# Kernel tuning notes

Hardware: AMD Instinct MI355X
Metric: run time of the kernel (lower is better)

## Reference

```python
import jax, jax.numpy as jnp
import numpy as np

DIM = 1024
HEADS = 16


def setup_inputs() -> dict:
    key = jax.random.key(0)
    ks = jax.random.split(key, 8)
    b, n, d = 2, 2048, DIM
    x = jax.random.normal(ks[0], (b, n, d), dtype=jnp.float32)
    # Linear(dim, 3*dim, bias=False): weight stored as [dim, 3*dim] (pre-transposed)
    W_qkv = jax.random.normal(ks[1], (d, 3 * d), dtype=jnp.float32) * (d ** -0.5)
    # Linear(dim, dim) with bias
    W_out = jax.random.normal(ks[2], (d, d), dtype=jnp.float32) * (d ** -0.5)
    b_out = jnp.zeros((d,), dtype=jnp.float32)
    alpha = jnp.ones((1,), dtype=jnp.float32)
    beta = jnp.zeros((1,), dtype=jnp.float32) + 0.5  # nonzero so softmax path is exercised
    gamma = jnp.zeros((1,), dtype=jnp.float32) + 0.1
    return {"x": x, "W_qkv": W_qkv, "W_out": W_out, "b_out": b_out,
            "alpha": alpha, "beta": beta, "gamma": gamma}


def reference(x, W_qkv, W_out, b_out, alpha, beta, gamma):
    b, n, d = x.shape
    h = HEADS
    hd = d // h
    scale = d ** -0.5  # note: full dim, as in the original module
    qkv = x @ W_qkv  # [b, n, 3d]
    q, k, v = jnp.split(qkv, 3, axis=-1)
    # [b, n, d] -> [b, h, n, hd]
    to_heads = lambda t: t.reshape(b, n, h, hd).transpose(0, 2, 1, 3)
    q, k, v = to_heads(q), to_heads(k), to_heads(v)
    dots = jnp.einsum("bhqd,bhkd->bhqk", q, k) * scale  # [b, h, n, n]
    attn = (alpha[0] * jnp.eye(n, dtype=x.dtype)
            + beta[0] * jax.nn.softmax(dots, axis=-1)
            - gamma[0] / n)
    out = jnp.einsum("bhqk,bhkd->bhqd", attn, v)  # [b, h, n, hd]
    out = out.transpose(0, 2, 1, 3).reshape(b, n, d)
    return out @ W_out + b_out
```

## Files before the change

### kernel.cpp

```cpp
#include <hip/hip_runtime.h>
#include <hip/hip_bf16.h>

#define DEVI __device__ __forceinline__

typedef __attribute__((ext_vector_type(8))) short bf16x8;
typedef __attribute__((ext_vector_type(4))) short bf16x4;
typedef __attribute__((ext_vector_type(4))) float f32x4;

DEVI unsigned short f2bf(float f) {
    unsigned u = __float_as_uint(f);
    u += 0x7FFF + ((u >> 16) & 1);
    return (unsigned short)(u >> 16);
}
DEVI float bf2f(unsigned short h) {
    return __uint_as_float(((unsigned)h) << 16);
}
DEVI f32x4 mfma16(bf16x8 a, bf16x8 b, f32x4 c) {
    return __builtin_amdgcn_mfma_f32_16x16x32_bf16(a, b, c, 0, 0, 0);
}
DEVI void gload_lds16(const void* g, void* l) {
    __builtin_amdgcn_global_load_lds(
        (const __attribute__((address_space(1))) unsigned int*)g,
        (__attribute__((address_space(3))) unsigned int*)l, 16, 0, 0);
}

DEVI void wt_body(const float* __restrict__ W, unsigned short* __restrict__ Wt,
                  int N, int n0, int k0, float sc, int tid,
                  unsigned short (*T)[72])
{
#pragma unroll
    for (int j = 0; j < 4; ++j) {
        int idx = tid + j * 256;
        int kk = idx >> 4, c4 = (idx & 15) << 2;
        float4 v = *(const float4*)(W + (size_t)(k0 + kk) * N + n0 + c4);
        T[c4 + 0][kk] = f2bf(v.x * sc); T[c4 + 1][kk] = f2bf(v.y * sc);
        T[c4 + 2][kk] = f2bf(v.z * sc); T[c4 + 3][kk] = f2bf(v.w * sc);
    }
    __syncthreads();
#pragma unroll
    for (int j = 0; j < 4; ++j) {
        int idx = tid + j * 256;
        int n = idx >> 4, c4 = (idx & 15) << 2;
        *(bf16x4*)(Wt + (size_t)(n0 + n) * 1024 + k0 + c4) = *(bf16x4*)&T[n][c4];
    }
}

__global__ __launch_bounds__(256) void k_prep(
    const float* __restrict__ X, const float* __restrict__ Wqkv,
    const float* __restrict__ Wout,
    unsigned short* __restrict__ Xb, unsigned short* __restrict__ Wt1,
    unsigned short* __restrict__ Wt2, float* __restrict__ vsum)
{
    __shared__ unsigned short T[64][72];
    const int tid = threadIdx.x;
    const int bid = blockIdx.x;
    const float QSC = 1.4426950408889634f / 32.0f;
    if (bid < 1024) {
        if (bid == 0) {
            float4 z = (float4){0.f, 0.f, 0.f, 0.f};
            ((float4*)vsum)[tid] = z;
            ((float4*)vsum)[tid + 256] = z;
        }
        int i = bid * 256 + tid;
#pragma unroll
        for (int j = 0; j < 4; ++j) {
            int idx = i + j * 262144;
            float4 v = *(const float4*)(X + (size_t)idx * 4);
            bf16x4 hv;
            hv[0] = (short)f2bf(v.x); hv[1] = (short)f2bf(v.y);
            hv[2] = (short)f2bf(v.z); hv[3] = (short)f2bf(v.w);
            *(bf16x4*)(Xb + (size_t)idx * 4) = hv;
        }
    } else if (bid < 1792) {
        int idx = bid - 1024;
        int n0 = (idx % 48) * 64, k0 = (idx / 48) * 64;
        wt_body(Wqkv, Wt1, 3072, n0, k0, (n0 < 1024) ? QSC : 1.0f, tid, T);
    } else {
        int idx = bid - 1792;
        int n0 = (idx & 15) * 64, k0 = (idx >> 4) * 64;
        wt_body(Wout, Wt2, 1024, n0, k0, 1.0f, tid, T);
    }
}

__global__ __launch_bounds__(256) void k_gemm1(
    const unsigned short* __restrict__ A, const unsigned short* __restrict__ B,
    unsigned short* __restrict__ C, unsigned short* __restrict__ Vt,
    float* __restrict__ vsum)
{
    __shared__ unsigned short Sh[18432];
    unsigned short* As = Sh;
    unsigned short* Bs = Sh + 8192;
    const int tid = threadIdx.x, lane = tid & 63, wid = tid >> 6;
    const int wr = (wid >> 1) * 64, wc = (wid & 1) * 64;
    const int row0 = blockIdx.y * 128, col0 = (23 - blockIdx.x) * 128;
    const int rsel = lane & 15, kgr = (lane >> 4) * 8;
    const int lr = lane >> 3, lc = (lane & 7) * 8;

    f32x4 acc[4][4];
#pragma unroll
    for (int i = 0; i < 4; ++i)
#pragma unroll
        for (int j = 0; j < 4; ++j) acc[i][j] = (f32x4){0.f, 0.f, 0.f, 0.f};

    for (int k0 = 0; k0 < 1024; k0 += 64) {
        __syncthreads();
#pragma unroll
        for (int i = 0; i < 4; ++i) {
            int rb = wid * 32 + i * 8;
            gload_lds16(A + (size_t)(row0 + rb + lr) * 1024 + k0 + lc, As + rb * 64);
            gload_lds16(B + (size_t)(col0 + rb + lr) * 1024 + k0 + lc, Bs + rb * 64);
        }
        __syncthreads();
#pragma unroll
        for (int ks = 0; ks < 2; ++ks) {
            bf16x8 a[4], b[4];
            int ko = ks * 32 + kgr;
#pragma unroll
            for (int mi = 0; mi < 4; ++mi)
                a[mi] = *(const bf16x8*)(As + (wr + mi * 16 + rsel) * 64 + ko);
#pragma unroll
            for (int nj = 0; nj < 4; ++nj)
                b[nj] = *(const bf16x8*)(Bs + (wc + nj * 16 + rsel) * 64 + ko);
#pragma unroll
            for (int mi = 0; mi < 4; ++mi)
#pragma unroll
                for (int nj = 0; nj < 4; ++nj)
                    acc[mi][nj] = mfma16(a[mi], b[nj], acc[mi][nj]);
        }
    }
    __syncthreads();
    unsigned short (*wb)[72] = (unsigned short (*)[72])(Sh + wid * 4608);
    const int g4 = (lane >> 4) << 2;
#pragma unroll
    for (int mi = 0; mi < 4; ++mi)
#pragma unroll
        for (int nj = 0; nj < 4; ++nj)
#pragma unroll
            for (int r = 0; r < 4; ++r)
                wb[mi * 16 + g4 + r][nj * 16 + rsel] = f2bf(acc[mi][nj][r]);
#pragma unroll
    for (int rr = 0; rr < 8; ++rr) {
        int row = rr * 8 + (lane >> 3);
        int c8 = (lane & 7) * 8;
        bf16x8 v = *(const bf16x8*)&wb[row][c8];
        *(bf16x8*)(C + (size_t)(row0 + wr + row) * 3072 + col0 + wc + c8) = v;
    }

    if (col0 >= 2048) {
        const int b_ = row0 >> 11;
        const int n0 = (row0 & 2047) + wr;
        const int bh = b_ * 16 + ((col0 + wc - 2048) >> 6);
#pragma unroll
        for (int nj = 0; nj < 4; ++nj) {
            float s = 0.f;
#pragma unroll
            for (int mi = 0; mi < 4; ++mi)
#pragma unroll
                for (int r = 0; r < 4; ++r) s += acc[mi][nj][r];
            s += __shfl_xor(s, 16);
            s += __shfl_xor(s, 32);
            if (lane < 16) atomicAdd(&vsum[bh * 64 + nj * 16 + rsel], s);
        }
        unsigned short* vtb = Vt + (size_t)bh * 64 * 2048 + n0 + lane;
#pragma unroll 8
        for (int dv = 0; dv < 64; ++dv)
            vtb[(size_t)dv * 2048] = wb[lane][dv];
    }
}

__global__ __launch_bounds__(256) void k_attn(
    const unsigned short* __restrict__ qkv, const unsigned short* __restrict__ Vt,
    const float* __restrict__ vsum,
    const float* __restrict__ alpha_p, const float* __restrict__ beta_p,
    const float* __restrict__ gamma_p,
    unsigned short* __restrict__ AO)
{
    __shared__ unsigned short Ks[4][64][64];
    __shared__ unsigned short Vs[4][64][64];
    __shared__ unsigned short Ps[4][32][64];
    const int tid = threadIdx.x, lane = tid & 63, wid = tid >> 6;
    const int swz = (blockIdx.x & 7) * 64 + (blockIdx.x >> 3);
    const int bh = swz >> 4, qtb = swz & 15;
    const int b = bh >> 4, h = bh & 15;
    const int q0 = qtb * 128;
    const int rsel = lane & 15, g = lane >> 4;
    const int g4 = g << 2;
    const int wq0 = wid * 32;
    const int r7 = rsel & 7;

    bf16x8 bq[2][2];
#pragma unroll
    for (int qt = 0; qt < 2; ++qt) {
        const unsigned short* qrow =
            qkv + (size_t)(b * 2048 + q0 + wq0 + qt * 16 + rsel) * 3072 + h * 64;
        bq[qt][0] = *(const bf16x8*)(qrow + g * 8);
        bq[qt][1] = *(const bf16x8*)(qrow + 32 + g * 8);
    }

    const int sr = lane >> 3;
    const int ss = (lane & 7) ^ sr;
    const int rb0 = wid * 16, rb1 = wid * 16 + 8;
    const unsigned short* kp0 = qkv + (size_t)(b * 2048) * 3072 + 1024 + h * 64
                              + (size_t)(rb0 + sr) * 3072 + ss * 8;
    const unsigned short* kp1 = kp0 + (size_t)8 * 3072;
    const unsigned short* vp0 = Vt + (size_t)bh * 64 * 2048
                              + (size_t)(rb0 + sr) * 2048 + ss * 8;
    const unsigned short* vp1 = vp0 + (size_t)8 * 2048;
    const size_t KADV = (size_t)64 * 3072;

    f32x4 o[2][4], ol[2];
#pragma unroll
    for (int qt = 0; qt < 2; ++qt) {
#pragma unroll
        for (int dj = 0; dj < 4; ++dj) o[qt][dj] = (f32x4){0.f, 0.f, 0.f, 0.f};
        ol[qt] = (f32x4){0.f, 0.f, 0.f, 0.f};
    }
    bf16x8 ones;
#pragma unroll
    for (int e = 0; e < 8; ++e) ones[e] = (short)0x3F80;

#define STAGE(BUF)                                                             \
    {                                                                          \
        gload_lds16(kp0, &Ks[BUF][rb0][0]);                                    \
        gload_lds16(kp1, &Ks[BUF][rb1][0]);                                    \
        gload_lds16(vp0, &Vs[BUF][rb0][0]);                                    \
        gload_lds16(vp1, &Vs[BUF][rb1][0]);                                    \
        kp0 += KADV; kp1 += KADV; vp0 += 64; vp1 += 64;                        \
    }

    STAGE(0); STAGE(1);
    asm volatile("s_waitcnt vmcnt(0)" ::: "memory");
    __syncthreads();

#define QK(CUR, S)                                                             \
    {                                                                          \
        _Pragma("unroll")                                                      \
        for (int qt = 0; qt < 2; ++qt)                                         \
            _Pragma("unroll")                                                  \
            for (int kj = 0; kj < 4; ++kj)                                     \
                S[qt][kj] = (f32x4){0.f, 0.f, 0.f, 0.f};                       \
        __builtin_amdgcn_s_setprio(1);                                         \
        _Pragma("unroll")                                                      \
        for (int ks = 0; ks < 2; ++ks) {                                       \
            const int sl = ((ks * 4 + g) ^ r7) * 8;                            \
            bf16x8 ak[4];                                                      \
            _Pragma("unroll")                                                  \
            for (int kj = 0; kj < 4; ++kj)                                     \
                ak[kj] = *(const bf16x8*)(&Ks[CUR][kj * 16 + rsel][sl]);       \
            _Pragma("unroll")                                                  \
            for (int qt = 0; qt < 2; ++qt)                                     \
                _Pragma("unroll")                                              \
                for (int kj = 0; kj < 4; ++kj)                                 \
                    S[qt][kj] = mfma16(ak[kj], bq[qt][ks], S[qt][kj]);         \
        }                                                                      \
        __builtin_amdgcn_s_setprio(0);                                         \
    }

#define EPV(CUR, S)                                                            \
    {                                                                          \
        _Pragma("unroll")                                                      \
        for (int qt = 0; qt < 2; ++qt)                                         \
            _Pragma("unroll")                                                  \
            for (int kj = 0; kj < 4; ++kj) {                                   \
                float p0 = __builtin_amdgcn_exp2f(S[qt][kj][0]);               \
                float p1 = __builtin_amdgcn_exp2f(S[qt][kj][1]);               \
                float p2 = __builtin_amdgcn_exp2f(S[qt][kj][2]);               \
                float p3 = __builtin_amdgcn_exp2f(S[qt][kj][3]);               \
                union { __hip_bfloat162 h2[2]; uint2 u; } pk;                  \
                pk.h2[0] = __float22bfloat162_rn(make_float2(p0, p1));         \
                pk.h2[1] = __float22bfloat162_rn(make_float2(p2, p3));         \
                const int slot16 = (kj * 2 + (g >> 1)) ^ r7;                   \
                *(uint2*)(&Ps[wid][qt * 16 + rsel][slot16 * 8 + (g & 1) * 4])  \
                    = pk.u;                                                    \
            }                                                                  \
        __builtin_amdgcn_s_setprio(1);                                         \
        _Pragma("unroll")                                                      \
        for (int ks = 0; ks < 2; ++ks) {                                       \
            const int sl = ((ks * 4 + g) ^ r7) * 8;                            \
            bf16x8 pa0 = *(const bf16x8*)(&Ps[wid][rsel][sl]);                 \
            bf16x8 pa1 = *(const bf16x8*)(&Ps[wid][16 + rsel][sl]);            \
            bf16x8 vb[4];                                                      \
            _Pragma("unroll")                                                  \
            for (int dj = 0; dj < 4; ++dj)                                     \
                vb[dj] = *(const bf16x8*)(&Vs[CUR][dj * 16 + rsel][sl]);       \
            _Pragma("unroll")                                                  \
            for (int dj = 0; dj < 4; ++dj) {                                   \
                o[0][dj] = mfma16(pa0, vb[dj], o[0][dj]);                      \
                o[1][dj] = mfma16(pa1, vb[dj], o[1][dj]);                      \
            }                                                                  \
            ol[0] = mfma16(pa0, ones, ol[0]);                                  \
            ol[1] = mfma16(pa1, ones, ol[1]);                                  \
        }                                                                      \
        __builtin_amdgcn_s_setprio(0);                                         \
    }

#define PAIR(C0, C1, DOPF)                                                     \
    {                                                                          \
        f32x4 s0[2][4], s1[2][4];                                              \
        if (DOPF) { STAGE(C0 ^ 2); STAGE(C1 ^ 2); }                            \
        QK(C0, s0);                                                            \
        QK(C1, s1);                                                            \
        EPV(C0, s0);                                                           \
        EPV(C1, s1);                                                           \
        asm volatile("s_waitcnt vmcnt(0)" ::: "memory");                       \
        __syncthreads();                                                       \
    }

#pragma unroll 1
    for (int i = 0; i < 8; ++i) {
        PAIR(0, 1, true);
        PAIR(2, 3, (i < 7));
    }
#undef PAIR
#undef EPV
#undef QK
#undef STAGE

    const float alpha = *alpha_p, beta = *beta_p;
    const float gn = (*gamma_p) / 2048.0f;
#pragma unroll
    for (int qt = 0; qt < 2; ++qt) {
        float linv[4];
#pragma unroll
        for (int r = 0; r < 4; ++r)
            linv[r] = beta / ol[qt][r];
#pragma unroll
        for (int dj = 0; dj < 4; ++dj)
#pragma unroll
            for (int r = 0; r < 4; ++r) {
                int qrow = q0 + wq0 + qt * 16 + g4 + r;
                int dv = dj * 16 + rsel;
                float ov = o[qt][dj][r] * linv[r];
                float vdiag = bf2f(qkv[(size_t)(b * 2048 + qrow) * 3072 + 2048 + h * 64 + dv]);
                float vs = vsum[bh * 64 + dv];
                float res = ov + alpha * vdiag - gn * vs;
                AO[(size_t)(b * 2048 + qrow) * 1024 + h * 64 + dv] = f2bf(res);
            }
    }
}

__global__ __launch_bounds__(256) void k_gemm2(
    const unsigned short* __restrict__ A, const unsigned short* __restrict__ B,
    const float* __restrict__ bias, float* __restrict__ Out)
{
    __shared__ unsigned short As[64 * 64];
    __shared__ unsigned short Bs[64 * 64];
    const int tid = threadIdx.x, lane = tid & 63, wid = tid >> 6;
    const int wr = (wid >> 1) * 32, wc = (wid & 1) * 32;
    const int row0 = blockIdx.y * 64, col0 = blockIdx.x * 64;
    const int rsel = lane & 15, kgr = (lane >> 4) * 8;
    const int lr = lane >> 3, lc = (lane & 7) * 8;

    f32x4 acc[2][2];
#pragma unroll
    for (int i = 0; i < 2; ++i)
#pragma unroll
        for (int j = 0; j < 2; ++j) acc[i][j] = (f32x4){0.f, 0.f, 0.f, 0.f};

    for (int k0 = 0; k0 < 1024; k0 += 64) {
        __syncthreads();
#pragma unroll
        for (int i = 0; i < 2; ++i) {
            int rb = wid * 16 + i * 8;
            gload_lds16(A + (size_t)(row0 + rb + lr) * 1024 + k0 + lc, As + rb * 64);
            gload_lds16(B + (size_t)(col0 + rb + lr) * 1024 + k0 + lc, Bs + rb * 64);
        }
        __syncthreads();
#pragma unroll
        for (int ks = 0; ks < 2; ++ks) {
            bf16x8 a[2], b[2];
            int ko = ks * 32 + kgr;
#pragma unroll
            for (int mi = 0; mi < 2; ++mi)
                a[mi] = *(const bf16x8*)(As + (wr + mi * 16 + rsel) * 64 + ko);
#pragma unroll
            for (int nj = 0; nj < 2; ++nj)
                b[nj] = *(const bf16x8*)(Bs + (wc + nj * 16 + rsel) * 64 + ko);
#pragma unroll
            for (int mi = 0; mi < 2; ++mi)
#pragma unroll
                for (int nj = 0; nj < 2; ++nj)
                    acc[mi][nj] = mfma16(a[mi], b[nj], acc[mi][nj]);
        }
    }
    const int rbase = row0 + wr + ((lane >> 4) << 2);
    const int cbase = col0 + wc + rsel;
#pragma unroll
    for (int mi = 0; mi < 2; ++mi)
#pragma unroll
        for (int nj = 0; nj < 2; ++nj) {
            int gc = cbase + nj * 16;
            float bv = bias[gc];
#pragma unroll
            for (int r = 0; r < 4; ++r)
                Out[(size_t)(rbase + mi * 16 + r) * 1024 + gc] = acc[mi][nj][r] + bv;
        }
}

extern "C" void kernel_launch(void* const* d_in, const int* in_sizes, int n_in,
                              void* d_out, int out_size, void* d_ws, size_t ws_size,
                              hipStream_t stream) {
    const float* x     = (const float*)d_in[0];
    const float* Wqkv  = (const float*)d_in[1];
    const float* Wout  = (const float*)d_in[2];
    const float* bout  = (const float*)d_in[3];
    const float* alpha = (const float*)d_in[4];
    const float* beta  = (const float*)d_in[5];
    const float* gamma = (const float*)d_in[6];
    float* out = (float*)d_out;

    char* ws = (char*)d_ws;
    unsigned short* Xb  = (unsigned short*)(ws);
    unsigned short* Wt1 = (unsigned short*)(ws + 8388608);
    unsigned short* Wt2 = (unsigned short*)(ws + 14680064);
    unsigned short* qkv = (unsigned short*)(ws + 16777216);
    unsigned short* Vt  = (unsigned short*)(ws + 41943040);
    float* vsum         = (float*)(ws + 50331648);
    unsigned short* AO  = Xb;

    k_prep<<<2048, 256, 0, stream>>>(x, Wqkv, Wout, Xb, Wt1, Wt2, vsum);
    k_gemm1<<<dim3(24, 32), 256, 0, stream>>>(Xb, Wt1, qkv, Vt, vsum);
    k_attn<<<512, 256, 0, stream>>>(qkv, Vt, vsum, alpha, beta, gamma, AO);
    k_gemm2<<<dim3(16, 64), 256, 0, stream>>>(AO, Wt2, bout, out);
}
```

Before: 133.0 us.

## Double-buffer LDS tiles in both projection GEMMs to overlap loads with MFMA

Result: faster. 122.1 us, median of 2 (-8.2%).

```diff
diff --git a/kernel.cpp b/kernel.cpp
--- a/kernel.cpp
+++ b/kernel.cpp
@@ -87,9 +87,7 @@
     unsigned short* __restrict__ C, unsigned short* __restrict__ Vt,
     float* __restrict__ vsum)
 {
-    __shared__ unsigned short Sh[18432];
-    unsigned short* As = Sh;
-    unsigned short* Bs = Sh + 8192;
+    __shared__ unsigned short Sh[32768];
     const int tid = threadIdx.x, lane = tid & 63, wid = tid >> 6;
     const int wr = (wid >> 1) * 64, wc = (wid & 1) * 64;
     const int row0 = blockIdx.y * 128, col0 = (23 - blockIdx.x) * 128;
@@ -102,32 +100,67 @@
 #pragma unroll
         for (int j = 0; j < 4; ++j) acc[i][j] = (f32x4){0.f, 0.f, 0.f, 0.f};
 
-    for (int k0 = 0; k0 < 1024; k0 += 64) {
-        __syncthreads();
-#pragma unroll
-        for (int i = 0; i < 4; ++i) {
-            int rb = wid * 32 + i * 8;
-            gload_lds16(A + (size_t)(row0 + rb + lr) * 1024 + k0 + lc, As + rb * 64);
-            gload_lds16(B + (size_t)(col0 + rb + lr) * 1024 + k0 + lc, Bs + rb * 64);
-        }
-        __syncthreads();
-#pragma unroll
-        for (int ks = 0; ks < 2; ++ks) {
-            bf16x8 a[4], b[4];
-            int ko = ks * 32 + kgr;
-#pragma unroll
-            for (int mi = 0; mi < 4; ++mi)
-                a[mi] = *(const bf16x8*)(As + (wr + mi * 16 + rsel) * 64 + ko);
-#pragma unroll
-            for (int nj = 0; nj < 4; ++nj)
-                b[nj] = *(const bf16x8*)(Bs + (wc + nj * 16 + rsel) * 64 + ko);
-#pragma unroll
-            for (int mi = 0; mi < 4; ++mi)
-#pragma unroll
-                for (int nj = 0; nj < 4; ++nj)
-                    acc[mi][nj] = mfma16(a[mi], b[nj], acc[mi][nj]);
-        }
-    }
+    const unsigned short* ap[4];
+    const unsigned short* bp[4];
+#pragma unroll
+    for (int i = 0; i < 4; ++i) {
+        ap[i] = A + (size_t)(row0 + wid * 32 + i * 8 + lr) * 1024 + lc;
+        bp[i] = B + (size_t)(col0 + wid * 32 + i * 8 + lr) * 1024 + lc;
+    }
+
+#define GSTAGE(BUF)                                                            \
+    {                                                                          \
+        _Pragma("unroll")                                                      \
+        for (int i = 0; i < 4; ++i) {                                          \
+            int rb = wid * 32 + i * 8;                                         \
+            gload_lds16(ap[i], Sh + (BUF) * 16384 + rb * 64);                  \
+            gload_lds16(bp[i], Sh + (BUF) * 16384 + 8192 + rb * 64);           \
+            ap[i] += 64; bp[i] += 64;                                          \
+        }                                                                      \
+    }
+
+#define GCOMP(CUR)                                                             \
+    {                                                                          \
+        const unsigned short* As_ = Sh + (CUR) * 16384;                        \
+        const unsigned short* Bs_ = As_ + 8192;                                \
+        _Pragma("unroll")                                                      \
+        for (int ks = 0; ks < 2; ++ks) {                                       \
+            bf16x8 a[4], b[4];                                                 \
+            int ko = ks * 32 + kgr;                                            \
+            _Pragma("unroll")                                                  \
+            for (int mi = 0; mi < 4; ++mi)                                     \
+                a[mi] = *(const bf16x8*)(As_ + (wr + mi * 16 + rsel) * 64 + ko);\
+            _Pragma("unroll")                                                  \
+            for (int nj = 0; nj < 4; ++nj)                                     \
+                b[nj] = *(const bf16x8*)(Bs_ + (wc + nj * 16 + rsel) * 64 + ko);\
+            _Pragma("unroll")                                                  \
+            for (int mi = 0; mi < 4; ++mi)                                     \
+                _Pragma("unroll")                                              \
+                for (int nj = 0; nj < 4; ++nj)                                 \
+                    acc[mi][nj] = mfma16(a[mi], b[nj], acc[mi][nj]);           \
+        }                                                                      \
+    }
+
+#define GBODY(CUR, DOPF)                                                       \
+    {                                                                          \
+        if (DOPF) GSTAGE((CUR) ^ 1);                                           \
+        GCOMP(CUR);                                                            \
+        asm volatile("s_waitcnt vmcnt(0)" ::: "memory");                       \
+        __syncthreads();                                                       \
+    }
+
+    GSTAGE(0);
+    asm volatile("s_waitcnt vmcnt(0)" ::: "memory");
+    __syncthreads();
+#pragma unroll 1
+    for (int i = 0; i < 8; ++i) {
+        GBODY(0, true);
+        GBODY(1, (i < 7));
+    }
+#undef GBODY
+#undef GCOMP
+#undef GSTAGE
+
     __syncthreads();
     unsigned short (*wb)[72] = (unsigned short (*)[72])(Sh + wid * 4608);
     const int g4 = (lane >> 4) << 2;
@@ -343,8 +376,7 @@
     const unsigned short* __restrict__ A, const unsigned short* __restrict__ B,
     const float* __restrict__ bias, float* __restrict__ Out)
 {
-    __shared__ unsigned short As[64 * 64];
-    __shared__ unsigned short Bs[64 * 64];
+    __shared__ unsigned short Sh[16384];
     const int tid = threadIdx.x, lane = tid & 63, wid = tid >> 6;
     const int wr = (wid >> 1) * 32, wc = (wid & 1) * 32;
     const int row0 = blockIdx.y * 64, col0 = blockIdx.x * 64;
@@ -357,32 +389,61 @@
 #pragma unroll
         for (int j = 0; j < 2; ++j) acc[i][j] = (f32x4){0.f, 0.f, 0.f, 0.f};
 
-    for (int k0 = 0; k0 < 1024; k0 += 64) {
-        __syncthreads();
-#pragma unroll
-        for (int i = 0; i < 2; ++i) {
-            int rb = wid * 16 + i * 8;
-            gload_lds16(A + (size_t)(row0 + rb + lr) * 1024 + k0 + lc, As + rb * 64);
-            gload_lds16(B + (size_t)(col0 + rb + lr) * 1024 + k0 + lc, Bs + rb * 64);
-        }
-        __syncthreads();
-#pragma unroll
-        for (int ks = 0; ks < 2; ++ks) {
-            bf16x8 a[2], b[2];
-            int ko = ks * 32 + kgr;
-#pragma unroll
-            for (int mi = 0; mi < 2; ++mi)
-                a[mi] = *(const bf16x8*)(As + (wr + mi * 16 + rsel) * 64 + ko);
-#pragma unroll
-            for (int nj = 0; nj < 2; ++nj)
-                b[nj] = *(const bf16x8*)(Bs + (wc + nj * 16 + rsel) * 64 + ko);
-#pragma unroll
-            for (int mi = 0; mi < 2; ++mi)
-#pragma unroll
-                for (int nj = 0; nj < 2; ++nj)
-                    acc[mi][nj] = mfma16(a[mi], b[nj], acc[mi][nj]);
-        }
-    }
+    const unsigned short* ap[2];
+    const unsigned short* bp[2];
+#pragma unroll
+    for (int i = 0; i < 2; ++i) {
+        ap[i] = A + (size_t)(row0 + wid * 16 + i * 8 + lr) * 1024 + lc;
+        bp[i] = B + (size_t)(col0 + wid * 16 + i * 8 + lr) * 1024 + lc;
+    }
+
+#define G2STAGE(BUF)                                                           \
+    {                                                                          \
+        _Pragma("unroll")                                                      \
+        for (int i = 0; i < 2; ++i) {                                          \
+            int rb = wid * 16 + i * 8;                                         \
+            gload_lds16(ap[i], Sh + (BUF) * 8192 + rb * 64);                   \
+            gload_lds16(bp[i], Sh + (BUF) * 8192 + 4096 + rb * 64);            \
+            ap[i] += 64; bp[i] += 64;                                          \
+        }                                                                      \
+    }
+
+#define G2BODY(CUR, DOPF)                                                      \
+    {                                                                          \
+        if (DOPF) G2STAGE((CUR) ^ 1);                                          \
+        const unsigned short* As_ = Sh + (CUR) * 8192;                         \
+        const unsigned short* Bs_ = As_ + 4096;                                \
+        _Pragma("unroll")                                                      \
+        for (int ks = 0; ks < 2; ++ks) {                                       \
+            bf16x8 a[2], b[2];                                                 \
+            int ko = ks * 32 + kgr;                                            \
+            _Pragma("unroll")                                                  \
+            for (int mi = 0; mi < 2; ++mi)                                     \
+                a[mi] = *(const bf16x8*)(As_ + (wr + mi * 16 + rsel) * 64 + ko);\
+            _Pragma("unroll")                                                  \
+            for (int nj = 0; nj < 2; ++nj)                                     \
+                b[nj] = *(const bf16x8*)(Bs_ + (wc + nj * 16 + rsel) * 64 + ko);\
+            _Pragma("unroll")                                                  \
+            for (int mi = 0; mi < 2; ++mi)                                     \
+                _Pragma("unroll")                                              \
+                for (int nj = 0; nj < 2; ++nj)                                 \
+                    acc[mi][nj] = mfma16(a[mi], b[nj], acc[mi][nj]);           \
+        }                                                                      \
+        asm volatile("s_waitcnt vmcnt(0)" ::: "memory");                       \
+        __syncthreads();                                                       \
+    }
+
+    G2STAGE(0);
+    asm volatile("s_waitcnt vmcnt(0)" ::: "memory");
+    __syncthreads();
+#pragma unroll 1
+    for (int i = 0; i < 8; ++i) {
+        G2BODY(0, true);
+        G2BODY(1, (i < 7));
+    }
+#undef G2BODY
+#undef G2STAGE
+
     const int rbase = row0 + wr + ((lane >> 4) << 2);
     const int cbase = col0 + wc + rsel;
 #pragma unroll
```
